# Optimization experiments

Hardware: AMD Instinct MI355X
Metric: run time of the kernel (lower is better)

The kernel has to match this reference:

```python
import jax, jax.numpy as jnp
import numpy as np

B = 4096          # graphs per batch
SENSORS = 9       # nodes per graph (9*8 = 72 directed edges = 36 pairs x 2)
PAIRS = 36
E_PER_G = 72
HID = 3.0  # unused marker
H = 128
L = 4
EPS = 1e-8


def _build_edge_index():
    # 36 unordered pairs (i<j); per pair emit (i->j) then (j->i) so that
    # reshape(B, 36, 2) groups the two directions of each pair together.
    pairs = [(i, j) for i in range(SENSORS) for j in range(i + 1, SENSORS)]
    rows, cols = [], []
    for i, j in pairs:
        rows += [i, j]
        cols += [j, i]
    rows = np.asarray(rows, np.int32)
    cols = np.asarray(cols, np.int32)
    offs = (np.arange(B, dtype=np.int32) * SENSORS)[:, None]  # [B,1]
    row = (rows[None, :] + offs).reshape(-1)
    col = (cols[None, :] + offs).reshape(-1)
    return jnp.asarray(np.stack([row, col]))  # [2, B*72]


def setup_inputs() -> dict:
    key = jax.random.key(0)
    ks = iter(jax.random.split(key, 32))
    N = B * SENSORS

    def lin(k, fin, fout):
        s = 1.0 / np.sqrt(fin)
        kw, kb = jax.random.split(k)
        return (jax.random.uniform(kw, (fin, fout), jnp.float32, -s, s),
                jax.random.uniform(kb, (fout,), jnp.float32, -s, s))

    x_nodes = jax.random.normal(next(ks), (N, 2), jnp.float32)
    damage_locs = jax.random.normal(next(ks), (B, 2), jnp.float32)
    edge_index = _build_edge_index()
    node_batch = jnp.repeat(jnp.arange(B, dtype=jnp.int32), SENSORS)

    enc_n_w, enc_n_b = lin(next(ks), 2, H)
    enc_e_w1, enc_e_b1 = lin(next(ks), 6, H)
    enc_e_w2, enc_e_b2 = lin(next(ks), H, H)

    ew1, eb1, ew2, eb2, nw1, nb1, nw2, nb2 = [], [], [], [], [], [], [], []
    for _ in range(L):
        w, b = lin(next(ks), 3 * H, H); ew1.append(w); eb1.append(b)
        w, b = lin(next(ks), H, H);     ew2.append(w); eb2.append(b)
        w, b = lin(next(ks), 2 * H, H); nw1.append(w); nb1.append(b)
        w, b = lin(next(ks), H, H);     nw2.append(w); nb2.append(b)
    stk = lambda xs: jnp.stack(xs)

    dec_w1, dec_b1 = lin(next(ks), H, H // 2)
    dec_w2, dec_b2 = lin(next(ks), H // 2, 1)

    return dict(
        x_nodes=x_nodes, damage_locs=damage_locs,
        enc_n_w=enc_n_w, enc_n_b=enc_n_b,
        enc_e_w1=enc_e_w1, enc_e_b1=enc_e_b1, enc_e_w2=enc_e_w2, enc_e_b2=enc_e_b2,
        edge_w1=stk(ew1), edge_b1=stk(eb1), edge_w2=stk(ew2), edge_b2=stk(eb2),
        node_w1=stk(nw1), node_b1=stk(nb1), node_w2=stk(nw2), node_b2=stk(nb2),
        dec_w1=dec_w1, dec_b1=dec_b1, dec_w2=dec_w2, dec_b2=dec_b2,
        edge_index=edge_index, node_batch=node_batch,
    )


def _forward(x_nodes, damage_locs,
             enc_n_w, enc_n_b, enc_e_w1, enc_e_b1, enc_e_w2, enc_e_b2,
             edge_w1, edge_b1, edge_w2, edge_b2,
             node_w1, node_b1, node_w2, node_b2,
             dec_w1, dec_b1, dec_w2, dec_b2,
             edge_index, node_batch):
    N = x_nodes.shape[0]
    row, col = edge_index[0], edge_index[1]
    src = x_nodes[row]                      # [E,2] sender coords (p1)
    dst = x_nodes[col]                      # [E,2] receiver coords (p2)
    dmg = damage_locs[node_batch[row]]      # [E,2] (p3)

    vec = src - dst
    edge_len = jnp.sqrt(jnp.sum(vec * vec, -1, keepdims=True) + EPS)
    d21 = dst - src
    l2 = jnp.clip(jnp.sum(d21 * d21, -1, keepdims=True), EPS, None)
    t = jnp.clip(jnp.sum((dmg - src) * d21, -1, keepdims=True) / l2, 0.0, 1.0)
    proj = src + t * d21
    d_path = jnp.sqrt(jnp.sum((dmg - proj) ** 2, -1, keepdims=True) + EPS)
    d_tx = jnp.sqrt(jnp.sum((src - dmg) ** 2, -1, keepdims=True) + EPS)
    d_rx = jnp.sqrt(jnp.sum((dst - dmg) ** 2, -1, keepdims=True) + EPS)
    phys = jnp.concatenate([vec, edge_len, d_path, d_tx, d_rx], axis=1)  # [E,6]

    h_n = x_nodes @ enc_n_w + enc_n_b
    h_e = jax.nn.relu(phys @ enc_e_w1 + enc_e_b1) @ enc_e_w2 + enc_e_b2

    ones = jnp.ones((row.shape[0],), h_n.dtype)
    deg = jnp.clip(jax.ops.segment_sum(ones, col, num_segments=N), 1.0, None)[:, None]

    for l in range(L):
        ein = jnp.concatenate([h_n[row], h_n[col], h_e], axis=1)  # [E,3H]
        h_e = h_e + jax.nn.relu(ein @ edge_w1[l] + edge_b1[l]) @ edge_w2[l] + edge_b2[l]
        # PyG default message(x_j): mean of sender node features at receiver
        agg = jax.ops.segment_sum(h_n[row], col, num_segments=N) / deg
        nin = jnp.concatenate([h_n, agg], axis=1)                 # [N,2H]
        h_n = h_n + jax.nn.relu(nin @ node_w1[l] + node_b1[l]) @ node_w2[l] + node_b2[l]

    dec = jax.nn.sigmoid(jax.nn.relu(h_e @ dec_w1 + dec_b1) @ dec_w2 + dec_b2)  # [E,1]
    return dec.reshape(B, PAIRS, 2).mean(axis=2)  # [B,36]


def reference(x_nodes, damage_locs,
              enc_n_w, enc_n_b, enc_e_w1, enc_e_b1, enc_e_w2, enc_e_b2,
              edge_w1, edge_b1, edge_w2, edge_b2,
              node_w1, node_b1, node_w2, node_b2,
              dec_w1, dec_b1, dec_w2, dec_b2,
              edge_index, node_batch):
    return _forward(x_nodes, damage_locs,
                    enc_n_w, enc_n_b, enc_e_w1, enc_e_b1, enc_e_w2, enc_e_b2,
                    edge_w1, edge_b1, edge_w2, edge_b2,
                    node_w1, node_b1, node_w2, node_b2,
                    dec_w1, dec_b1, dec_w2, dec_b2,
                    edge_index, node_batch)
```

## Files before the change

kernel.cpp:

```cpp
#include <hip/hip_runtime.h>
#include <math.h>

typedef unsigned short u16;
typedef __attribute__((ext_vector_type(8))) short bf16x8;
typedef __attribute__((ext_vector_type(4))) float f32x4;

#define NSENS 9
#define NEDGE 72
#define NPAIR 36
#define HDIM 128
#define NLAYER 4
#define FEPS 1e-8f

#define ST    136
#define STNIN 264
#define STPH  40

__device__ __forceinline__ u16 f2bf(float f) {
    unsigned u = __float_as_uint(f);
    return (u16)((u + 0x7FFFu + ((u >> 16) & 1u)) >> 16);
}
__device__ __forceinline__ float bf2f(u16 h) { return __uint_as_float(((unsigned)h) << 16); }

#define SZ_EE1 (1*8*512)
#define SZ_EE2 (4*8*512)
#define SZ_EW1 (12*8*512)
#define SZ_EW2 (4*8*512)
#define SZ_NW1 (8*8*512)
#define SZ_NW2 (4*8*512)
#define SZ_DW1 (4*4*512)
#define OFF_EE1 0
#define OFF_EE2 (OFF_EE1 + SZ_EE1)
#define OFF_EW1 (OFF_EE2 + SZ_EE2)
#define OFF_EW2 (OFF_EW1 + 4*SZ_EW1)
#define OFF_NW1 (OFF_EW2 + 4*SZ_EW2)
#define OFF_NW2 (OFF_NW1 + 4*SZ_NW1)
#define OFF_DW1 (OFF_NW2 + 4*SZ_NW2)

__global__ void pack_w(const float* __restrict__ src, u16* __restrict__ dst,
                       int Ksrc, int N, int NT, int ls, int ld) {
    const int l  = blockIdx.y;
    const int kb = blockIdx.x / NT, nt = blockIdx.x % NT;
    const int ln = threadIdx.x, q = ln >> 4, c = ln & 15;
    const int n  = nt * 16 + c;
    const float* s = src + l * ls;
    u16* d = dst + l * ld + ((kb * NT + nt) * 64 + ln) * 8;
#pragma unroll
    for (int j = 0; j < 8; ++j) {
        int k = kb * 32 + q * 8 + j;
        d[j] = f2bf((k < Ksrc) ? s[k * N + n] : 0.f);
    }
}

template<int NMT, int NKB, int NT, typename FA>
__device__ __forceinline__ void wave_gemm(const u16* __restrict__ Wp, int nt, int ln,
                                          FA fa, f32x4* acc) {
    const u16* wp = Wp + (nt * 64 + ln) * 8;
#pragma unroll
    for (int kb = 0; kb < NKB; ++kb) {
        bf16x8 b = *(const bf16x8*)(wp + kb * NT * 512);
#pragma unroll
        for (int mt = 0; mt < NMT; ++mt) {
            bf16x8 a = fa(mt, kb);
            acc[mt] = __builtin_amdgcn_mfma_f32_16x16x32_bf16(a, b, acc[mt], 0, 0, 0);
        }
    }
}

#define ZACC(A, N) do { _Pragma("unroll") for (int _i = 0; _i < (N); ++_i) \
                        (A)[_i] = (f32x4){0.f, 0.f, 0.f, 0.f}; } while (0)

extern "C" __global__ void __launch_bounds__(512, 2)
gnn_mfma(const float* __restrict__ x_nodes, const float* __restrict__ damage_locs,
         const float* __restrict__ enc_n_w, const float* __restrict__ enc_n_b,
         const float* __restrict__ enc_e_b1, const float* __restrict__ enc_e_b2,
         const float* __restrict__ edge_b1, const float* __restrict__ edge_b2,
         const float* __restrict__ node_b1, const float* __restrict__ node_b2,
         const float* __restrict__ dec_b1, const float* __restrict__ dec_w2,
         const float* __restrict__ dec_b2,
         const u16* __restrict__ wpack, float* __restrict__ out)
{
    __shared__ __align__(16) u16 b_he[80 * ST];
    __shared__ __align__(16) u16 b_t [80 * ST];
    __shared__ __align__(16) u16 b_hn[16 * ST];
    __shared__ __align__(16) u16 b_nt[16 * ST];
    __shared__ __align__(16) u16 b_nin[16 * STNIN];
    __shared__ __align__(16) u16 b_ph[80 * STPH];
    __shared__ float s_x[NSENS * 2];
    __shared__ float s_dmg[2];
    __shared__ float s_val[NEDGE];
    __shared__ int s_src[NEDGE], s_dst[NEDGE];

    const int g   = blockIdx.x;
    const int tid = threadIdx.x;
    const int wv  = tid >> 6, ln = tid & 63;
    const int q   = ln >> 4,  cl = ln & 15;
    const int col = wv * 16 + cl;

    for (int i = tid; i < 80 * ST; i += 512) { b_he[i] = 0; b_t[i] = 0; }
    for (int i = tid; i < 16 * ST; i += 512) { b_hn[i] = 0; b_nt[i] = 0; }
    for (int i = tid; i < 16 * STNIN; i += 512) b_nin[i] = 0;
    for (int i = tid; i < 80 * STPH;  i += 512) b_ph[i] = 0;
    if (tid < NSENS * 2) s_x[tid] = x_nodes[g * NSENS * 2 + tid];
    if (tid < 2)         s_dmg[tid] = damage_locs[g * 2 + tid];
    if (tid < NEDGE) {
        int p = tid >> 1;
        int i = 0, rem = p, cnt = 8;
        while (rem >= cnt) { rem -= cnt; --cnt; ++i; }
        int j = i + 1 + rem;
        s_src[tid] = (tid & 1) ? j : i;
        s_dst[tid] = (tid & 1) ? i : j;
    }
    __syncthreads();

    if (tid < NEDGE) {
        const int si = s_src[tid], di = s_dst[tid];
        const float sx = s_x[2*si], sy = s_x[2*si+1];
        const float dx = s_x[2*di], dy = s_x[2*di+1];
        const float gx = s_dmg[0],  gy = s_dmg[1];
        const float vx = sx - dx, vy = sy - dy;
        const float vv = vx*vx + vy*vy;
        const float elen = sqrtf(vv + FEPS);
        const float l2 = fmaxf(vv, FEPS);
        float t = ((gx - sx) * (dx - sx) + (gy - sy) * (dy - sy)) / l2;
        t = fminf(fmaxf(t, 0.f), 1.f);
        const float px = sx + t * (dx - sx), py = sy + t * (dy - sy);
        u16* ph = b_ph + tid * STPH;
        ph[0] = f2bf(vx); ph[1] = f2bf(vy); ph[2] = f2bf(elen);
        ph[3] = f2bf(sqrtf((gx-px)*(gx-px) + (gy-py)*(gy-py) + FEPS));
        ph[4] = f2bf(sqrtf((sx-gx)*(sx-gx) + (sy-gy)*(sy-gy) + FEPS));
        ph[5] = f2bf(sqrtf((dx-gx)*(dx-gx) + (dy-gy)*(dy-gy) + FEPS));
    }

    f32x4 m_hn;
    {
        const float w0 = enc_n_w[col], w1 = enc_n_w[HDIM + col], bb = enc_n_b[col];
#pragma unroll
        for (int r = 0; r < 4; ++r) {
            const int R = q * 4 + r;
            float v = (R < NSENS) ? fmaf(s_x[2*R], w0, fmaf(s_x[2*R+1], w1, bb)) : 0.f;
            m_hn[r] = v;
            b_hn[R * ST + col] = f2bf(v);
        }
    }
    __syncthreads();

    int rowS[5], rowD[5], rowE[5];
#pragma unroll
    for (int mt = 0; mt < 5; ++mt) {
        int e = mt * 16 + cl; if (e >= NEDGE) e = NEDGE - 1;
        rowS[mt] = s_src[e] * ST; rowD[mt] = s_dst[e] * ST; rowE[mt] = e * ST;
    }

    auto fa_t   = [&](int mt, int kb) -> bf16x8 {
        return *(const bf16x8*)(b_t + (mt * 16 + cl) * ST + kb * 32 + q * 8); };
    auto fa_he  = [&](int mt, int kb) -> bf16x8 {
        return *(const bf16x8*)(b_he + (mt * 16 + cl) * ST + kb * 32 + q * 8); };
    auto fa_ph  = [&](int mt, int kb) -> bf16x8 {
        return *(const bf16x8*)(b_ph + (mt * 16 + cl) * STPH + q * 8); };
    auto fa_nin = [&](int mt, int kb) -> bf16x8 {
        return *(const bf16x8*)(b_nin + cl * STNIN + kb * 32 + q * 8); };
    auto fa_nt  = [&](int mt, int kb) -> bf16x8 {
        return *(const bf16x8*)(b_nt + cl * ST + kb * 32 + q * 8); };
    auto fa_ein = [&](int mt, int kb) -> bf16x8 {
        const u16* p;
        if (kb < 4)      p = b_hn + rowS[mt] + kb * 32;
        else if (kb < 8) p = b_hn + rowD[mt] + (kb - 4) * 32;
        else             p = b_he + rowE[mt] + (kb - 8) * 32;
        return *(const bf16x8*)(p + q * 8); };

    f32x4 m_he[5];

    {
        f32x4 acc[5]; ZACC(acc, 5);
        wave_gemm<5, 1, 8>(wpack + OFF_EE1, wv, ln, fa_ph, acc);
        const float bb = enc_e_b1[col];
#pragma unroll
        for (int mt = 0; mt < 5; ++mt)
#pragma unroll
            for (int r = 0; r < 4; ++r) {
                const int R = mt * 16 + q * 4 + r;
                if (R < NEDGE) b_t[R * ST + col] = f2bf(fmaxf(acc[mt][r] + bb, 0.f));
            }
    }
    __syncthreads();
    {
        f32x4 acc[5]; ZACC(acc, 5);
        wave_gemm<5, 4, 8>(wpack + OFF_EE2, wv, ln, fa_t, acc);
        const float bb = enc_e_b2[col];
#pragma unroll
        for (int mt = 0; mt < 5; ++mt)
#pragma unroll
            for (int r = 0; r < 4; ++r) {
                const int R = mt * 16 + q * 4 + r;
                m_he[mt][r] = acc[mt][r] + bb;
                if (R < NEDGE) b_he[R * ST + col] = f2bf(m_he[mt][r]);
            }
    }
    __syncthreads();

    for (int l = 0; l < NLAYER; ++l) {
        {
            f32x4 acc[5]; ZACC(acc, 5);
            wave_gemm<5, 12, 8>(wpack + OFF_EW1 + l * SZ_EW1, wv, ln, fa_ein, acc);
            const float bb = edge_b1[l * HDIM + col];
#pragma unroll
            for (int mt = 0; mt < 5; ++mt)
#pragma unroll
                for (int r = 0; r < 4; ++r) {
                    const int R = mt * 16 + q * 4 + r;
                    if (R < NEDGE) b_t[R * ST + col] = f2bf(fmaxf(acc[mt][r] + bb, 0.f));
                }
        }
        __syncthreads();
        {
            f32x4 acc[5]; ZACC(acc, 5);
            wave_gemm<5, 4, 8>(wpack + OFF_EW2 + l * SZ_EW2, wv, ln, fa_t, acc);
            const float bb = edge_b2[l * HDIM + col];
#pragma unroll
            for (int mt = 0; mt < 5; ++mt)
#pragma unroll
                for (int r = 0; r < 4; ++r) {
                    const int R = mt * 16 + q * 4 + r;
                    m_he[mt][r] += acc[mt][r] + bb;
                    if (R < NEDGE) b_he[R * ST + col] = f2bf(m_he[mt][r]);
                }
        }
        __syncthreads();
        {
            float p4 = m_hn[0] + m_hn[1] + m_hn[2] + m_hn[3];
            p4 += __shfl_xor(p4, 16);
            p4 += __shfl_xor(p4, 32);
#pragma unroll
            for (int r = 0; r < 4; ++r) {
                const int R = q * 4 + r;
                if (R < NSENS) {
                    b_nin[R * STNIN + col]        = f2bf(m_hn[r]);
                    b_nin[R * STNIN + HDIM + col] = f2bf((p4 - m_hn[r]) * 0.125f);
                }
            }
        }
        __syncthreads();
        {
            f32x4 acc[1]; ZACC(acc, 1);
            wave_gemm<1, 8, 8>(wpack + OFF_NW1 + l * SZ_NW1, wv, ln, fa_nin, acc);
            const float bb = node_b1[l * HDIM + col];
#pragma unroll
            for (int r = 0; r < 4; ++r) {
                const int R = q * 4 + r;
                b_nt[R * ST + col] = f2bf(fmaxf(acc[0][r] + bb, 0.f));
            }
        }
        __syncthreads();
        {
            f32x4 acc[1]; ZACC(acc, 1);
            wave_gemm<1, 4, 8>(wpack + OFF_NW2 + l * SZ_NW2, wv, ln, fa_nt, acc);
            const float bb = node_b2[l * HDIM + col];
#pragma unroll
            for (int r = 0; r < 4; ++r) {
                const int R = q * 4 + r;
                if (R < NSENS) {
                    m_hn[r] += acc[0][r] + bb;
                    b_hn[R * ST + col] = f2bf(m_hn[r]);
                }
            }
        }
        __syncthreads();
    }

    {
        const int ntd = wv & 3;
        const int mt0 = (wv < 4) ? 0 : 2;
        f32x4 acc[3]; ZACC(acc, 3);
        auto fa_d = [&](int mt, int kb) -> bf16x8 {
            return *(const bf16x8*)(b_he + ((mt0 + mt) * 16 + cl) * ST + kb * 32 + q * 8); };
        wave_gemm<3, 4, 4>(wpack + OFF_DW1, ntd, ln, fa_d, acc);
        const int c64 = ntd * 16 + cl;
        const float bb = dec_b1[c64];
#pragma unroll
        for (int mt = 0; mt < 3; ++mt)
#pragma unroll
            for (int r = 0; r < 4; ++r) {
                const int R = (mt0 + mt) * 16 + q * 4 + r;
                if (R < NEDGE) b_t[R * ST + c64] = f2bf(fmaxf(acc[mt][r] + bb, 0.f));
            }
    }
    __syncthreads();
    if (tid < NEDGE) {
        float a = dec_b2[0];
        const u16* tt = b_t + tid * ST;
#pragma unroll
        for (int k = 0; k < 64; ++k) a = fmaf(bf2f(tt[k]), dec_w2[k], a);
        s_val[tid] = 1.f / (1.f + expf(-a));
    }
    __syncthreads();
    if (tid < NPAIR)
        out[g * NPAIR + tid] = 0.5f * (s_val[2 * tid] + s_val[2 * tid + 1]);
}

extern "C" void kernel_launch(void* const* d_in, const int* in_sizes, int n_in,
                              void* d_out, int out_size, void* d_ws, size_t ws_size,
                              hipStream_t stream) {
    const float* x_nodes     = (const float*)d_in[0];
    const float* damage_locs = (const float*)d_in[1];
    const float* enc_n_w  = (const float*)d_in[2];
    const float* enc_n_b  = (const float*)d_in[3];
    const float* enc_e_w1 = (const float*)d_in[4];
    const float* enc_e_b1 = (const float*)d_in[5];
    const float* enc_e_w2 = (const float*)d_in[6];
    const float* enc_e_b2 = (const float*)d_in[7];
    const float* edge_w1  = (const float*)d_in[8];
    const float* edge_b1  = (const float*)d_in[9];
    const float* edge_w2  = (const float*)d_in[10];
    const float* edge_b2  = (const float*)d_in[11];
    const float* node_w1  = (const float*)d_in[12];
    const float* node_b1  = (const float*)d_in[13];
    const float* node_w2  = (const float*)d_in[14];
    const float* node_b2  = (const float*)d_in[15];
    const float* dec_w1   = (const float*)d_in[16];
    const float* dec_b1   = (const float*)d_in[17];
    const float* dec_w2   = (const float*)d_in[18];
    const float* dec_b2   = (const float*)d_in[19];
    float* out = (float*)d_out;
    u16* ws = (u16*)d_ws;

    hipLaunchKernelGGL(pack_w, dim3(1*8, 1),  dim3(64), 0, stream, enc_e_w1, ws + OFF_EE1, 6,   128, 8, 0, 0);
    hipLaunchKernelGGL(pack_w, dim3(4*8, 1),  dim3(64), 0, stream, enc_e_w2, ws + OFF_EE2, 128, 128, 8, 0, 0);
    hipLaunchKernelGGL(pack_w, dim3(12*8, 4), dim3(64), 0, stream, edge_w1,  ws + OFF_EW1, 384, 128, 8, 384*128, SZ_EW1);
    hipLaunchKernelGGL(pack_w, dim3(4*8, 4),  dim3(64), 0, stream, edge_w2,  ws + OFF_EW2, 128, 128, 8, 128*128, SZ_EW2);
    hipLaunchKernelGGL(pack_w, dim3(8*8, 4),  dim3(64), 0, stream, node_w1,  ws + OFF_NW1, 256, 128, 8, 256*128, SZ_NW1);
    hipLaunchKernelGGL(pack_w, dim3(4*8, 4),  dim3(64), 0, stream, node_w2,  ws + OFF_NW2, 128, 128, 8, 128*128, SZ_NW2);
    hipLaunchKernelGGL(pack_w, dim3(4*4, 1),  dim3(64), 0, stream, dec_w1,   ws + OFF_DW1, 128, 64,  4, 0, 0);

    const int ngraph = in_sizes[1] / 2;
    hipLaunchKernelGGL(gnn_mfma, dim3(ngraph), dim3(512), 0, stream,
                       x_nodes, damage_locs, enc_n_w, enc_n_b,
                       enc_e_b1, enc_e_b2, edge_b1, edge_b2,
                       node_b1, node_b2, dec_b1, dec_w2, dec_b2,
                       ws, out);
}
```

Measured before the change: 430.7 us.

## Merge weight-pack launches, alias LDS buffers, and pack bf16 stores via lane shuffles

Folds the seven weight-packing kernels into one launch to cut launch overhead. Shrinks LDS by aliasing the phi and node-input buffers onto the edge buffers and zeroing with 16-byte stores, which could raise occupancy. Replaces scalar 16-bit LDS stores of MFMA outputs with a shuffle-based transpose that writes two bf16 values per 32-bit store. One barrier is also moved later. Aliasing relies on the phi and node-input buffers being dead at the points where the edge buffers are overwritten.

```diff
diff --git a/kernel.cpp b/kernel.cpp
--- a/kernel.cpp
+++ b/kernel.cpp
@@ -21,6 +21,9 @@
     return (u16)((u + 0x7FFFu + ((u >> 16) & 1u)) >> 16);
 }
 __device__ __forceinline__ float bf2f(u16 h) { return __uint_as_float(((unsigned)h) << 16); }
+__device__ __forceinline__ unsigned pkbf(float lo, float hi) {
+    return ((unsigned)f2bf(hi) << 16) | (unsigned)f2bf(lo);
+}
 
 #define SZ_EE1 (1*8*512)
 #define SZ_EE2 (4*8*512)
@@ -37,19 +40,41 @@
 #define OFF_NW2 (OFF_NW1 + 4*SZ_NW1)
 #define OFF_DW1 (OFF_NW2 + 4*SZ_NW2)
 
-__global__ void pack_w(const float* __restrict__ src, u16* __restrict__ dst,
-                       int Ksrc, int N, int NT, int ls, int ld) {
-    const int l  = blockIdx.y;
-    const int kb = blockIdx.x / NT, nt = blockIdx.x % NT;
+__device__ __forceinline__ void pack_one(const float* __restrict__ s, u16* __restrict__ d,
+                                         int Ksrc, int N, int NT, int kbnt) {
+    const int kb = kbnt / NT, nt = kbnt % NT;
     const int ln = threadIdx.x, q = ln >> 4, c = ln & 15;
     const int n  = nt * 16 + c;
-    const float* s = src + l * ls;
-    u16* d = dst + l * ld + ((kb * NT + nt) * 64 + ln) * 8;
+    u16* dp = d + ((kb * NT + nt) * 64 + ln) * 8;
 #pragma unroll
     for (int j = 0; j < 8; ++j) {
         int k = kb * 32 + q * 8 + j;
-        d[j] = f2bf((k < Ksrc) ? s[k * N + n] : 0.f);
-    }
+        dp[j] = f2bf((k < Ksrc) ? s[k * N + n] : 0.f);
+    }
+}
+
+__global__ void pack_all(const float* __restrict__ ee1, const float* __restrict__ ee2,
+                         const float* __restrict__ ew1, const float* __restrict__ ew2,
+                         const float* __restrict__ nw1, const float* __restrict__ nw2,
+                         const float* __restrict__ dw1, u16* __restrict__ ws) {
+    int b = blockIdx.x;
+    if (b < 8)        { pack_one(ee1, ws + OFF_EE1, 6, 128, 8, b); return; }
+    b -= 8;
+    if (b < 32)       { pack_one(ee2, ws + OFF_EE2, 128, 128, 8, b); return; }
+    b -= 32;
+    if (b < 384)      { int l = b / 96;
+                        pack_one(ew1 + l*384*128, ws + OFF_EW1 + l*SZ_EW1, 384, 128, 8, b % 96); return; }
+    b -= 384;
+    if (b < 128)      { int l = b / 32;
+                        pack_one(ew2 + l*128*128, ws + OFF_EW2 + l*SZ_EW2, 128, 128, 8, b % 32); return; }
+    b -= 128;
+    if (b < 256)      { int l = b / 64;
+                        pack_one(nw1 + l*256*128, ws + OFF_NW1 + l*SZ_NW1, 256, 128, 8, b % 64); return; }
+    b -= 256;
+    if (b < 128)      { int l = b / 32;
+                        pack_one(nw2 + l*128*128, ws + OFF_NW2 + l*SZ_NW2, 128, 128, 8, b % 32); return; }
+    b -= 128;
+    pack_one(dw1, ws + OFF_DW1, 128, 64, 4, b);
 }
 
 template<int NMT, int NKB, int NT, typename FA>
@@ -80,16 +105,18 @@
          const float* __restrict__ dec_b2,
          const u16* __restrict__ wpack, float* __restrict__ out)
 {
-    __shared__ __align__(16) u16 b_he[80 * ST];
-    __shared__ __align__(16) u16 b_t [80 * ST];
-    __shared__ __align__(16) u16 b_hn[16 * ST];
-    __shared__ __align__(16) u16 b_nt[16 * ST];
-    __shared__ __align__(16) u16 b_nin[16 * STNIN];
-    __shared__ __align__(16) u16 b_ph[80 * STPH];
+    __shared__ __align__(16) u16 smem[192 * ST];
     __shared__ float s_x[NSENS * 2];
     __shared__ float s_dmg[2];
     __shared__ float s_val[NEDGE];
     __shared__ int s_src[NEDGE], s_dst[NEDGE];
+
+    u16* b_he  = smem;
+    u16* b_t   = smem + 80 * ST;
+    u16* b_hn  = smem + 160 * ST;
+    u16* b_nt  = smem + 176 * ST;
+    u16* b_ph  = b_he;
+    u16* b_nin = b_t;
 
     const int g   = blockIdx.x;
     const int tid = threadIdx.x;
@@ -97,10 +124,24 @@
     const int q   = ln >> 4,  cl = ln & 15;
     const int col = wv * 16 + cl;
 
-    for (int i = tid; i < 80 * ST; i += 512) { b_he[i] = 0; b_t[i] = 0; }
-    for (int i = tid; i < 16 * ST; i += 512) { b_hn[i] = 0; b_nt[i] = 0; }
-    for (int i = tid; i < 16 * STNIN; i += 512) b_nin[i] = 0;
-    for (int i = tid; i < 80 * STPH;  i += 512) b_ph[i] = 0;
+    auto stp = [&](u16* buf, int stride, int c, int Rb, int Rlim,
+                   float v0, float v1, float v2, float v3) {
+        const bool od = cl & 1;
+        float x = od ? v0 : v2, y = od ? v1 : v3;
+        float px = __shfl_xor(x, 1), py = __shfl_xor(y, 1);
+        float lo0 = od ? px : v0, hi0 = od ? v2 : px;
+        float lo1 = od ? py : v1, hi1 = od ? v3 : py;
+        const int r0 = Rb + (od ? 2 : 0);
+        const int cc = c & ~1;
+        if (r0 < Rlim)     *(unsigned*)(buf + r0 * stride + cc)       = pkbf(lo0, hi0);
+        if (r0 + 1 < Rlim) *(unsigned*)(buf + (r0 + 1) * stride + cc) = pkbf(lo1, hi1);
+    };
+
+    {
+        uint4 z = {0, 0, 0, 0};
+        uint4* zp = (uint4*)smem;
+        for (int i = tid; i < (192 * ST * 2) / 16; i += 512) zp[i] = z;
+    }
     if (tid < NSENS * 2) s_x[tid] = x_nodes[g * NSENS * 2 + tid];
     if (tid < 2)         s_dmg[tid] = damage_locs[g * 2 + tid];
     if (tid < NEDGE) {
@@ -138,12 +179,10 @@
 #pragma unroll
         for (int r = 0; r < 4; ++r) {
             const int R = q * 4 + r;
-            float v = (R < NSENS) ? fmaf(s_x[2*R], w0, fmaf(s_x[2*R+1], w1, bb)) : 0.f;
-            m_hn[r] = v;
-            b_hn[R * ST + col] = f2bf(v);
-        }
-    }
-    __syncthreads();
+            m_hn[r] = (R < NSENS) ? fmaf(s_x[2*R], w0, fmaf(s_x[2*R+1], w1, bb)) : 0.f;
+        }
+        stp(b_hn, ST, col, q * 4, NSENS, m_hn[0], m_hn[1], m_hn[2], m_hn[3]);
+    }
 
     int rowS[5], rowD[5], rowE[5];
 #pragma unroll
@@ -151,11 +190,10 @@
         int e = mt * 16 + cl; if (e >= NEDGE) e = NEDGE - 1;
         rowS[mt] = s_src[e] * ST; rowD[mt] = s_dst[e] * ST; rowE[mt] = e * ST;
     }
+    __syncthreads();
 
     auto fa_t   = [&](int mt, int kb) -> bf16x8 {
         return *(const bf16x8*)(b_t + (mt * 16 + cl) * ST + kb * 32 + q * 8); };
-    auto fa_he  = [&](int mt, int kb) -> bf16x8 {
-        return *(const bf16x8*)(b_he + (mt * 16 + cl) * ST + kb * 32 + q * 8); };
     auto fa_ph  = [&](int mt, int kb) -> bf16x8 {
         return *(const bf16x8*)(b_ph + (mt * 16 + cl) * STPH + q * 8); };
     auto fa_nin = [&](int mt, int kb) -> bf16x8 {
@@ -177,11 +215,9 @@
         const float bb = enc_e_b1[col];
 #pragma unroll
         for (int mt = 0; mt < 5; ++mt)
-#pragma unroll
-            for (int r = 0; r < 4; ++r) {
-                const int R = mt * 16 + q * 4 + r;
-                if (R < NEDGE) b_t[R * ST + col] = f2bf(fmaxf(acc[mt][r] + bb, 0.f));
-            }
+            stp(b_t, ST, col, mt * 16 + q * 4, NEDGE,
+                fmaxf(acc[mt][0] + bb, 0.f), fmaxf(acc[mt][1] + bb, 0.f),
+                fmaxf(acc[mt][2] + bb, 0.f), fmaxf(acc[mt][3] + bb, 0.f));
     }
     __syncthreads();
     {
@@ -189,13 +225,12 @@
         wave_gemm<5, 4, 8>(wpack + OFF_EE2, wv, ln, fa_t, acc);
         const float bb = enc_e_b2[col];
 #pragma unroll
-        for (int mt = 0; mt < 5; ++mt)
-#pragma unroll
-            for (int r = 0; r < 4; ++r) {
-                const int R = mt * 16 + q * 4 + r;
-                m_he[mt][r] = acc[mt][r] + bb;
-                if (R < NEDGE) b_he[R * ST + col] = f2bf(m_he[mt][r]);
-            }
+        for (int mt = 0; mt < 5; ++mt) {
+#pragma unroll
+            for (int r = 0; r < 4; ++r) m_he[mt][r] = acc[mt][r] + bb;
+            stp(b_he, ST, col, mt * 16 + q * 4, NEDGE,
+                m_he[mt][0], m_he[mt][1], m_he[mt][2], m_he[mt][3]);
+        }
     }
     __syncthreads();
 
@@ -206,11 +241,9 @@
             const float bb = edge_b1[l * HDIM + col];
 #pragma unroll
             for (int mt = 0; mt < 5; ++mt)
-#pragma unroll
-                for (int r = 0; r < 4; ++r) {
-                    const int R = mt * 16 + q * 4 + r;
-                    if (R < NEDGE) b_t[R * ST + col] = f2bf(fmaxf(acc[mt][r] + bb, 0.f));
-                }
+                stp(b_t, ST, col, mt * 16 + q * 4, NEDGE,
+                    fmaxf(acc[mt][0] + bb, 0.f), fmaxf(acc[mt][1] + bb, 0.f),
+                    fmaxf(acc[mt][2] + bb, 0.f), fmaxf(acc[mt][3] + bb, 0.f));
         }
         __syncthreads();
         {
@@ -218,38 +251,31 @@
             wave_gemm<5, 4, 8>(wpack + OFF_EW2 + l * SZ_EW2, wv, ln, fa_t, acc);
             const float bb = edge_b2[l * HDIM + col];
 #pragma unroll
-            for (int mt = 0; mt < 5; ++mt)
-#pragma unroll
-                for (int r = 0; r < 4; ++r) {
-                    const int R = mt * 16 + q * 4 + r;
-                    m_he[mt][r] += acc[mt][r] + bb;
-                    if (R < NEDGE) b_he[R * ST + col] = f2bf(m_he[mt][r]);
-                }
+            for (int mt = 0; mt < 5; ++mt) {
+#pragma unroll
+                for (int r = 0; r < 4; ++r) m_he[mt][r] += acc[mt][r] + bb;
+                stp(b_he, ST, col, mt * 16 + q * 4, NEDGE,
+                    m_he[mt][0], m_he[mt][1], m_he[mt][2], m_he[mt][3]);
+            }
         }
         __syncthreads();
         {
             float p4 = m_hn[0] + m_hn[1] + m_hn[2] + m_hn[3];
             p4 += __shfl_xor(p4, 16);
             p4 += __shfl_xor(p4, 32);
-#pragma unroll
-            for (int r = 0; r < 4; ++r) {
-                const int R = q * 4 + r;
-                if (R < NSENS) {
-                    b_nin[R * STNIN + col]        = f2bf(m_hn[r]);
-                    b_nin[R * STNIN + HDIM + col] = f2bf((p4 - m_hn[r]) * 0.125f);
-                }
-            }
+            stp(b_nin, STNIN, col, q * 4, NSENS, m_hn[0], m_hn[1], m_hn[2], m_hn[3]);
+            stp(b_nin, STNIN, HDIM + col, q * 4, NSENS,
+                (p4 - m_hn[0]) * 0.125f, (p4 - m_hn[1]) * 0.125f,
+                (p4 - m_hn[2]) * 0.125f, (p4 - m_hn[3]) * 0.125f);
         }
         __syncthreads();
         {
             f32x4 acc[1]; ZACC(acc, 1);
             wave_gemm<1, 8, 8>(wpack + OFF_NW1 + l * SZ_NW1, wv, ln, fa_nin, acc);
             const float bb = node_b1[l * HDIM + col];
-#pragma unroll
-            for (int r = 0; r < 4; ++r) {
-                const int R = q * 4 + r;
-                b_nt[R * ST + col] = f2bf(fmaxf(acc[0][r] + bb, 0.f));
-            }
+            stp(b_nt, ST, col, q * 4, 16,
+                fmaxf(acc[0][0] + bb, 0.f), fmaxf(acc[0][1] + bb, 0.f),
+                fmaxf(acc[0][2] + bb, 0.f), fmaxf(acc[0][3] + bb, 0.f));
         }
         __syncthreads();
         {
@@ -257,13 +283,9 @@
             wave_gemm<1, 4, 8>(wpack + OFF_NW2 + l * SZ_NW2, wv, ln, fa_nt, acc);
             const float bb = node_b2[l * HDIM + col];
 #pragma unroll
-            for (int r = 0; r < 4; ++r) {
-                const int R = q * 4 + r;
-                if (R < NSENS) {
-                    m_hn[r] += acc[0][r] + bb;
-                    b_hn[R * ST + col] = f2bf(m_hn[r]);
-                }
-            }
+            for (int r = 0; r < 4; ++r)
+                if (q * 4 + r < NSENS) m_hn[r] += acc[0][r] + bb;
+            stp(b_hn, ST, col, q * 4, NSENS, m_hn[0], m_hn[1], m_hn[2], m_hn[3]);
         }
         __syncthreads();
     }
@@ -279,11 +301,9 @@
         const float bb = dec_b1[c64];
 #pragma unroll
         for (int mt = 0; mt < 3; ++mt)
-#pragma unroll
-            for (int r = 0; r < 4; ++r) {
-                const int R = (mt0 + mt) * 16 + q * 4 + r;
-                if (R < NEDGE) b_t[R * ST + c64] = f2bf(fmaxf(acc[mt][r] + bb, 0.f));
-            }
+            stp(b_t, ST, c64, (mt0 + mt) * 16 + q * 4, NEDGE,
+                fmaxf(acc[mt][0] + bb, 0.f), fmaxf(acc[mt][1] + bb, 0.f),
+                fmaxf(acc[mt][2] + bb, 0.f), fmaxf(acc[mt][3] + bb, 0.f));
     }
     __syncthreads();
     if (tid < NEDGE) {
@@ -324,13 +344,8 @@
     float* out = (float*)d_out;
     u16* ws = (u16*)d_ws;
 
-    hipLaunchKernelGGL(pack_w, dim3(1*8, 1),  dim3(64), 0, stream, enc_e_w1, ws + OFF_EE1, 6,   128, 8, 0, 0);
-    hipLaunchKernelGGL(pack_w, dim3(4*8, 1),  dim3(64), 0, stream, enc_e_w2, ws + OFF_EE2, 128, 128, 8, 0, 0);
-    hipLaunchKernelGGL(pack_w, dim3(12*8, 4), dim3(64), 0, stream, edge_w1,  ws + OFF_EW1, 384, 128, 8, 384*128, SZ_EW1);
-    hipLaunchKernelGGL(pack_w, dim3(4*8, 4),  dim3(64), 0, stream, edge_w2,  ws + OFF_EW2, 128, 128, 8, 128*128, SZ_EW2);
-    hipLaunchKernelGGL(pack_w, dim3(8*8, 4),  dim3(64), 0, stream, node_w1,  ws + OFF_NW1, 256, 128, 8, 256*128, SZ_NW1);
-    hipLaunchKernelGGL(pack_w, dim3(4*8, 4),  dim3(64), 0, stream, node_w2,  ws + OFF_NW2, 128, 128, 8, 128*128, SZ_NW2);
-    hipLaunchKernelGGL(pack_w, dim3(4*4, 1),  dim3(64), 0, stream, dec_w1,   ws + OFF_DW1, 128, 64,  4, 0, 0);
+    hipLaunchKernelGGL(pack_all, dim3(952), dim3(64), 0, stream,
+                       enc_e_w1, enc_e_w2, edge_w1, edge_w2, node_w1, node_w2, dec_w1, ws);
 
     const int ngraph = in_sizes[1] / 2;
     hipLaunchKernelGGL(gnn_mfma, dim3(ngraph), dim3(512), 0, stream,
```

New measurement: 402.2 us. 6.6% less time.
